# Performance work log

Measured on AMD Instinct MI355X. Metric: run time of the kernel, lower is better.

## Reference

```python
import jax, jax.numpy as jnp
import numpy as np

B, S, H = 8, 2048, 1024

def setup_inputs() -> dict:
    key = jax.random.key(0)
    k1, k2, k3 = jax.random.split(key, 3)
    lstm_out = jax.random.normal(k1, (B, S, H), dtype=jnp.float32)
    # nn.Linear(hidden_size, hidden_size): weight [H, H], bias [H]
    W = jax.random.normal(k2, (H, H), dtype=jnp.float32) * (1.0 / np.sqrt(H))
    b = jax.random.normal(k3, (H,), dtype=jnp.float32) * 0.01
    return {"lstm_out": lstm_out, "W": W, "b": b}

def reference(lstm_out, W, b):
    # out = linear(lstm_out)  (torch Linear: x @ W.T + b)
    out = jnp.einsum('bsh,oh->bso', lstm_out, W) + b            # [B,S,H]
    # score = bmm(out, out^T)  -- unscaled, Q = K
    score = jnp.einsum('bqh,bkh->bqk', out, out)                # [B,S,S]
    attn = jax.nn.softmax(score, axis=-1)                       # [B,S,S]
    # context = bmm(attn, lstm_out)
    context = jnp.einsum('bqk,bkh->bqh', attn, lstm_out)        # [B,S,H]
    return context
```

## Files before the change

### kernel.cpp

```cpp
#include <hip/hip_runtime.h>
#include <hip/hip_bf16.h>
#include <stdint.h>

#define BB 8
#define SS 2048
#define HH 1024

typedef __bf16 bf16_t;
typedef bf16_t bf16x8 __attribute__((ext_vector_type(8)));
typedef float f32x4 __attribute__((ext_vector_type(4)));
typedef unsigned short u16x8 __attribute__((ext_vector_type(8)));

__device__ __forceinline__ unsigned short f2bf(float f) {
    unsigned int u = __float_as_uint(f);
    u += 0x7fffu + ((u >> 16) & 1u);
    return (unsigned short)(u >> 16);
}

__global__ __launch_bounds__(256) void cast_f32_bf16(
    const float* __restrict__ in, unsigned short* __restrict__ out, int n4)
{
    int i = blockIdx.x * blockDim.x + threadIdx.x;
    int stride = gridDim.x * blockDim.x;
    for (; i < n4; i += stride) {
        float4 v = reinterpret_cast<const float4*>(in)[i];
        ushort4 o;
        o.x = f2bf(v.x); o.y = f2bf(v.y); o.z = f2bf(v.z); o.w = f2bf(v.w);
        reinterpret_cast<ushort4*>(out)[i] = o;
    }
}

__global__ __launch_bounds__(256) void transpose_cast(
    const float* __restrict__ in,
    unsigned short* __restrict__ outN,
    unsigned short* __restrict__ outT)
{
    __shared__ float tile[32][33];
    const int tx = threadIdx.x, ty = threadIdx.y;
    const int h0 = blockIdx.x * 32, s0 = blockIdx.y * 32, b = blockIdx.z;
    const float* src = in + ((size_t)b * SS + s0) * HH + h0;
    unsigned short* dN = outN + ((size_t)b * SS + s0) * HH + h0;
    unsigned short* dT = outT + ((size_t)b * HH + h0) * SS + s0;
#pragma unroll
    for (int i = 0; i < 4; i++) {
        float v = src[(size_t)(ty + i * 8) * HH + tx];
        tile[ty + i * 8][tx] = v;
        dN[(size_t)(ty + i * 8) * HH + tx] = f2bf(v);
    }
    __syncthreads();
#pragma unroll
    for (int i = 0; i < 4; i++) {
        dT[(size_t)(ty + i * 8) * SS + tx] = f2bf(tile[tx][ty + i * 8]);
    }
}

__global__ __launch_bounds__(256) void softmax_rows(float* __restrict__ score)
{
    const size_t row = blockIdx.x;
    float* srow = score + row * 2048;
    const int t = threadIdx.x;
    const int wave = t >> 6, lane = t & 63;

    float4 v0 = reinterpret_cast<float4*>(srow)[t * 2];
    float4 v1 = reinterpret_cast<float4*>(srow)[t * 2 + 1];
    float x[8] = {v0.x, v0.y, v0.z, v0.w, v1.x, v1.y, v1.z, v1.w};

    float m = x[0];
#pragma unroll
    for (int i = 1; i < 8; i++) m = fmaxf(m, x[i]);
#pragma unroll
    for (int off = 32; off; off >>= 1) m = fmaxf(m, __shfl_xor(m, off));

    __shared__ float red[4];
    if (!lane) red[wave] = m;
    __syncthreads();
    m = fmaxf(fmaxf(red[0], red[1]), fmaxf(red[2], red[3]));

    float e[8];
    float s = 0.0f;
#pragma unroll
    for (int i = 0; i < 8; i++) { e[i] = __expf(x[i] - m); s += e[i]; }
#pragma unroll
    for (int off = 32; off; off >>= 1) s += __shfl_xor(s, off);
    __syncthreads();
    if (!lane) red[wave] = s;
    __syncthreads();
    s = red[0] + red[1] + red[2] + red[3];
    const float inv = 1.0f / s;

    unsigned short* drow = reinterpret_cast<unsigned short*>(score) + row * 4096 + (size_t)t * 8;
    u16x8 o;
#pragma unroll
    for (int i = 0; i < 8; i++) o[i] = f2bf(e[i] * inv);
    *reinterpret_cast<u16x8*>(drow) = o;
}

#define GLL16(gp, lp)                                                        \
    __builtin_amdgcn_global_load_lds(                                        \
        (const __attribute__((address_space(1))) unsigned int*)(gp),         \
        (__attribute__((address_space(3))) unsigned int*)(lp), 16, 0, 0)

template <int OUT_BF16, int HAS_BIAS>
__global__ __launch_bounds__(256) void gemm_nt(
    const unsigned short* __restrict__ A, long long aBatch, int lda,
    const unsigned short* __restrict__ Bmat, long long bBatch, int ldb,
    void* __restrict__ Cp, long long cBatch, int ldc,
    const float* __restrict__ bias, int K)
{
    __shared__ unsigned short As[128 * 32];
    __shared__ unsigned short Bs[128 * 32];

    const int tid = threadIdx.x;
    const int wave = tid >> 6, lane = tid & 63;
    const int wr = wave >> 1, wc = wave & 1;
    const int fr = lane & 15;
    const int fk = (lane >> 4) * 8;

    const unsigned short* Ab = A + (size_t)blockIdx.z * aBatch
        + ((size_t)blockIdx.y * 128 + wave * 32 + (lane >> 2)) * lda + (lane & 3) * 8;
    const unsigned short* Bb = Bmat + (size_t)blockIdx.z * bBatch
        + ((size_t)blockIdx.x * 128 + wave * 32 + (lane >> 2)) * ldb + (lane & 3) * 8;
    unsigned short* lA0 = As + (wave * 32) * 32;
    unsigned short* lA1 = As + (wave * 32 + 16) * 32;
    unsigned short* lB0 = Bs + (wave * 32) * 32;
    unsigned short* lB1 = Bs + (wave * 32 + 16) * 32;
    const size_t a16 = (size_t)16 * lda, b16 = (size_t)16 * ldb;

    f32x4 acc[4][4];
    const f32x4 zero = {0.0f, 0.0f, 0.0f, 0.0f};
#pragma unroll
    for (int m = 0; m < 4; m++)
#pragma unroll
        for (int n = 0; n < 4; n++) acc[m][n] = zero;

    for (int k0 = 0; k0 < K; k0 += 32) {
        GLL16(Ab + k0, lA0);
        GLL16(Ab + k0 + a16, lA1);
        GLL16(Bb + k0, lB0);
        GLL16(Bb + k0 + b16, lB1);
        __syncthreads();

        bf16x8 aF[4], bF[4];
#pragma unroll
        for (int m = 0; m < 4; m++)
            aF[m] = *reinterpret_cast<const bf16x8*>(As + (wr * 64 + m * 16 + fr) * 32 + fk);
#pragma unroll
        for (int n = 0; n < 4; n++)
            bF[n] = *reinterpret_cast<const bf16x8*>(Bs + (wc * 64 + n * 16 + fr) * 32 + fk);
#pragma unroll
        for (int m = 0; m < 4; m++)
#pragma unroll
            for (int n = 0; n < 4; n++)
                acc[m][n] = __builtin_amdgcn_mfma_f32_16x16x32_bf16(aF[m], bF[n], acc[m][n], 0, 0, 0);
        __syncthreads();
    }

    const int rBase = blockIdx.y * 128 + wr * 64 + (lane >> 4) * 4;
    const int cBase = blockIdx.x * 128 + wc * 64 + fr;
    if (OUT_BF16) {
        unsigned short* C = (unsigned short*)Cp + (size_t)blockIdx.z * cBatch;
#pragma unroll
        for (int n = 0; n < 4; n++) {
            const int col = cBase + n * 16;
            const float bv = HAS_BIAS ? bias[col] : 0.0f;
#pragma unroll
            for (int m = 0; m < 4; m++) {
                const int row = rBase + m * 16;
#pragma unroll
                for (int j = 0; j < 4; j++)
                    C[(size_t)(row + j) * ldc + col] = f2bf(acc[m][n][j] + bv);
            }
        }
    } else {
        float* C = (float*)Cp + (size_t)blockIdx.z * cBatch;
#pragma unroll
        for (int n = 0; n < 4; n++) {
            const int col = cBase + n * 16;
#pragma unroll
            for (int m = 0; m < 4; m++) {
                const int row = rBase + m * 16;
#pragma unroll
                for (int j = 0; j < 4; j++)
                    C[(size_t)(row + j) * ldc + col] = acc[m][n][j];
            }
        }
    }
}

extern "C" void kernel_launch(void* const* d_in, const int* in_sizes, int n_in,
                              void* d_out, int out_size, void* d_ws, size_t ws_size,
                              hipStream_t stream)
{
    const float* lstm = (const float*)d_in[0];
    const float* W    = (const float*)d_in[1];
    const float* bias = (const float*)d_in[2];
    float* out = (float*)d_out;

    unsigned short* lstm_bf = (unsigned short*)d_ws;
    unsigned short* out_bf  = lstm_bf + (size_t)BB * SS * HH;
    unsigned short* lstmT   = out_bf + (size_t)BB * SS * HH;
    unsigned short* W_bf    = lstmT + (size_t)BB * HH * SS;
    float* score            = (float*)(W_bf + (size_t)HH * HH);

    transpose_cast<<<dim3(HH / 32, SS / 32, BB), dim3(32, 8), 0, stream>>>(
        lstm, lstm_bf, lstmT);

    cast_f32_bf16<<<dim3(512), dim3(256), 0, stream>>>(W, W_bf, HH * HH / 4);

    gemm_nt<1, 1><<<dim3(HH / 128, BB * SS / 128, 1), dim3(256), 0, stream>>>(
        lstm_bf, 0, HH, W_bf, 0, HH, out_bf, 0, HH, bias, HH);

    gemm_nt<0, 0><<<dim3(SS / 128, SS / 128, BB), dim3(256), 0, stream>>>(
        out_bf, (long long)SS * HH, HH,
        out_bf, (long long)SS * HH, HH,
        score, (long long)SS * SS, SS, nullptr, HH);

    softmax_rows<<<dim3(BB * SS), dim3(256), 0, stream>>>(score);

    gemm_nt<0, 0><<<dim3(HH / 128, SS / 128, BB), dim3(256), 0, stream>>>(
        (const unsigned short*)score, (long long)SS * 4096, 4096,
        lstmT, (long long)HH * SS, SS,
        out, (long long)SS * HH, HH, nullptr, SS);
}
```

Measured before the change: 428.2 us.

## Use 256x256 triple-buffered GEMM tiles and store scores in bf16

Replaces the 128x128 single-buffered GEMM with a 256x256-tile, 512-thread kernel. It uses triple-buffered LDS prefetch via global_load_lds, an XOR-swizzled LDS layout, split MFMA phases with setprio, and an XCD-aware workgroup remap. The score matrix is now written directly in bf16, which halves the score write and softmax read traffic. This trades score precision before softmax (bf16 logits can have large magnitude) and higher register/LDS pressure for better data reuse and load/compute overlap.

```diff
diff --git a/kernel.cpp b/kernel.cpp
--- a/kernel.cpp
+++ b/kernel.cpp
@@ -15,6 +15,9 @@
     unsigned int u = __float_as_uint(f);
     u += 0x7fffu + ((u >> 16) & 1u);
     return (unsigned short)(u >> 16);
+}
+__device__ __forceinline__ float bf2f(unsigned short h) {
+    return __uint_as_float((unsigned int)h << 16);
 }
 
 __global__ __launch_bounds__(256) void cast_f32_bf16(
@@ -54,16 +57,17 @@
     }
 }
 
-__global__ __launch_bounds__(256) void softmax_rows(float* __restrict__ score)
+__global__ __launch_bounds__(256) void softmax_rows_bf16(unsigned short* __restrict__ score)
 {
     const size_t row = blockIdx.x;
-    float* srow = score + row * 2048;
+    unsigned short* srow = score + row * 2048;
     const int t = threadIdx.x;
     const int wave = t >> 6, lane = t & 63;
 
-    float4 v0 = reinterpret_cast<float4*>(srow)[t * 2];
-    float4 v1 = reinterpret_cast<float4*>(srow)[t * 2 + 1];
-    float x[8] = {v0.x, v0.y, v0.z, v0.w, v1.x, v1.y, v1.z, v1.w};
+    u16x8 v = *reinterpret_cast<u16x8*>(srow + (size_t)t * 8);
+    float x[8];
+#pragma unroll
+    for (int i = 0; i < 8; i++) x[i] = bf2f(v[i]);
 
     float m = x[0];
 #pragma unroll
@@ -88,11 +92,10 @@
     s = red[0] + red[1] + red[2] + red[3];
     const float inv = 1.0f / s;
 
-    unsigned short* drow = reinterpret_cast<unsigned short*>(score) + row * 4096 + (size_t)t * 8;
     u16x8 o;
 #pragma unroll
     for (int i = 0; i < 8; i++) o[i] = f2bf(e[i] * inv);
-    *reinterpret_cast<u16x8*>(drow) = o;
+    *reinterpret_cast<u16x8*>(srow + (size_t)t * 8) = o;
 }
 
 #define GLL16(gp, lp)                                                        \
@@ -101,62 +104,116 @@
         (__attribute__((address_space(3))) unsigned int*)(lp), 16, 0, 0)
 
 template <int OUT_BF16, int HAS_BIAS>
-__global__ __launch_bounds__(256) void gemm_nt(
+__global__ __launch_bounds__(512, 2) void gemm_nt_256(
     const unsigned short* __restrict__ A, long long aBatch, int lda,
-    const unsigned short* __restrict__ Bmat, long long bBatch, int ldb,
+    const unsigned short* __restrict__ Bm, long long bBatch, int ldb,
     void* __restrict__ Cp, long long cBatch, int ldc,
-    const float* __restrict__ bias, int K)
-{
-    __shared__ unsigned short As[128 * 32];
-    __shared__ unsigned short Bs[128 * 32];
+    const float* __restrict__ bias, int K, int GXT)
+{
+    __shared__ unsigned short lds[3 * 16384];
 
     const int tid = threadIdx.x;
     const int wave = tid >> 6, lane = tid & 63;
-    const int wr = wave >> 1, wc = wave & 1;
-    const int fr = lane & 15;
-    const int fk = (lane >> 4) * 8;
-
-    const unsigned short* Ab = A + (size_t)blockIdx.z * aBatch
-        + ((size_t)blockIdx.y * 128 + wave * 32 + (lane >> 2)) * lda + (lane & 3) * 8;
-    const unsigned short* Bb = Bmat + (size_t)blockIdx.z * bBatch
-        + ((size_t)blockIdx.x * 128 + wave * 32 + (lane >> 2)) * ldb + (lane & 3) * 8;
-    unsigned short* lA0 = As + (wave * 32) * 32;
-    unsigned short* lA1 = As + (wave * 32 + 16) * 32;
-    unsigned short* lB0 = Bs + (wave * 32) * 32;
-    unsigned short* lB1 = Bs + (wave * 32 + 16) * 32;
-    const size_t a16 = (size_t)16 * lda, b16 = (size_t)16 * ldb;
-
-    f32x4 acc[4][4];
+    const int wr = wave >> 2, wc = wave & 3;
+    const int fr = lane & 15, fc = lane >> 4;
+
+    const int q = gridDim.x >> 3;
+    const int x = blockIdx.x;
+    const int wgid = (x & 7) * q + (x >> 3);
+    const int bx = wgid % GXT, by = wgid / GXT;
+
+    const unsigned short* Ap = A + (size_t)blockIdx.z * aBatch + (size_t)by * 256 * lda;
+    const unsigned short* Bp = Bm + (size_t)blockIdx.z * bBatch + (size_t)bx * 256 * ldb;
+
+    const int sr = tid >> 2;
+    const int sc = tid & 3;
+    const int r0 = sr, r1 = sr + 128;
+    const unsigned short* sA0 = Ap + (size_t)r0 * lda + ((sc ^ ((r0 >> 1) & 3)) << 3);
+    const unsigned short* sA1 = Ap + (size_t)r1 * lda + ((sc ^ ((r1 >> 1) & 3)) << 3);
+    const unsigned short* sB0 = Bp + (size_t)r0 * ldb + ((sc ^ ((r0 >> 1) & 3)) << 3);
+    const unsigned short* sB1 = Bp + (size_t)r1 * ldb + ((sc ^ ((r1 >> 1) & 3)) << 3);
+    const int dA0 = wave * 512;
+    const int dA1 = 4096 + wave * 512;
+
+    const int kch = ((fc ^ ((fr >> 1) & 3)) << 3);
+    int offA[8], offB[4];
+#pragma unroll
+    for (int m = 0; m < 8; m++) offA[m] = (wr * 128 + m * 16 + fr) * 32 + kch;
+#pragma unroll
+    for (int n = 0; n < 4; n++) offB[n] = (wc * 64 + n * 16 + fr) * 32 + kch;
+
+    f32x4 acc[8][4];
     const f32x4 zero = {0.0f, 0.0f, 0.0f, 0.0f};
 #pragma unroll
-    for (int m = 0; m < 4; m++)
+    for (int m = 0; m < 8; m++)
 #pragma unroll
         for (int n = 0; n < 4; n++) acc[m][n] = zero;
 
-    for (int k0 = 0; k0 < K; k0 += 32) {
-        GLL16(Ab + k0, lA0);
-        GLL16(Ab + k0 + a16, lA1);
-        GLL16(Bb + k0, lB0);
-        GLL16(Bb + k0 + b16, lB1);
-        __syncthreads();
-
-        bf16x8 aF[4], bF[4];
-#pragma unroll
-        for (int m = 0; m < 4; m++)
-            aF[m] = *reinterpret_cast<const bf16x8*>(As + (wr * 64 + m * 16 + fr) * 32 + fk);
+    const int NT = K >> 5;
+
+    {
+        unsigned short* b0 = lds;
+        unsigned short* b1 = lds + 16384;
+        GLL16(sA0, b0 + dA0); GLL16(sA1, b0 + dA1);
+        GLL16(sB0, b0 + 8192 + dA0); GLL16(sB1, b0 + 8192 + dA1);
+        GLL16(sA0 + 32, b1 + dA0); GLL16(sA1 + 32, b1 + dA1);
+        GLL16(sB0 + 32, b1 + 8192 + dA0); GLL16(sB1 + 32, b1 + 8192 + dA1);
+    }
+    asm volatile("s_waitcnt vmcnt(4)" ::: "memory");
+    __builtin_amdgcn_sched_barrier(0);
+    __builtin_amdgcn_s_barrier();
+
+    for (int t = 0; t < NT; ++t) {
+        const int cur = t % 3;
+        const int nb = (t + 2) % 3;
+        const int sk = (t + 2 < NT ? t + 2 : NT - 1) << 5;
+        const unsigned short* tA = lds + cur * 16384;
+        const unsigned short* tB = tA + 8192;
+        unsigned short* nA = lds + nb * 16384;
+        unsigned short* nB = nA + 8192;
+
+        bf16x8 a0[4], b0[4];
+#pragma unroll
+        for (int m = 0; m < 4; m++)
+            a0[m] = *reinterpret_cast<const bf16x8*>(tA + offA[m]);
 #pragma unroll
         for (int n = 0; n < 4; n++)
-            bF[n] = *reinterpret_cast<const bf16x8*>(Bs + (wc * 64 + n * 16 + fr) * 32 + fk);
+            b0[n] = *reinterpret_cast<const bf16x8*>(tB + offB[n]);
+        GLL16(sA0 + sk, nA + dA0);
+        GLL16(sA1 + sk, nA + dA1);
+        __builtin_amdgcn_s_barrier();
+        __builtin_amdgcn_s_setprio(1);
 #pragma unroll
         for (int m = 0; m < 4; m++)
 #pragma unroll
             for (int n = 0; n < 4; n++)
-                acc[m][n] = __builtin_amdgcn_mfma_f32_16x16x32_bf16(aF[m], bF[n], acc[m][n], 0, 0, 0);
-        __syncthreads();
-    }
-
-    const int rBase = blockIdx.y * 128 + wr * 64 + (lane >> 4) * 4;
-    const int cBase = blockIdx.x * 128 + wc * 64 + fr;
+                acc[m][n] = __builtin_amdgcn_mfma_f32_16x16x32_bf16(a0[m], b0[n], acc[m][n], 0, 0, 0);
+        __builtin_amdgcn_s_setprio(0);
+        __builtin_amdgcn_s_barrier();
+
+        bf16x8 a1[4];
+#pragma unroll
+        for (int m = 0; m < 4; m++)
+            a1[m] = *reinterpret_cast<const bf16x8*>(tA + offA[4 + m]);
+        GLL16(sB0 + sk, nB + dA0);
+        GLL16(sB1 + sk, nB + dA1);
+        __builtin_amdgcn_s_barrier();
+        __builtin_amdgcn_s_setprio(1);
+#pragma unroll
+        for (int m = 0; m < 4; m++)
+#pragma unroll
+            for (int n = 0; n < 4; n++)
+                acc[4 + m][n] = __builtin_amdgcn_mfma_f32_16x16x32_bf16(a1[m], b0[n], acc[4 + m][n], 0, 0, 0);
+        __builtin_amdgcn_s_setprio(0);
+        asm volatile("s_waitcnt vmcnt(4)" ::: "memory");
+        __builtin_amdgcn_sched_barrier(0);
+        __builtin_amdgcn_s_barrier();
+    }
+    asm volatile("s_waitcnt vmcnt(0)" ::: "memory");
+    __builtin_amdgcn_sched_barrier(0);
+
+    const int rBase = by * 256 + wr * 128 + fc * 4;
+    const int cBase = bx * 256 + wc * 64 + fr;
     if (OUT_BF16) {
         unsigned short* C = (unsigned short*)Cp + (size_t)blockIdx.z * cBatch;
 #pragma unroll
@@ -164,7 +221,7 @@
             const int col = cBase + n * 16;
             const float bv = HAS_BIAS ? bias[col] : 0.0f;
 #pragma unroll
-            for (int m = 0; m < 4; m++) {
+            for (int m = 0; m < 8; m++) {
                 const int row = rBase + m * 16;
 #pragma unroll
                 for (int j = 0; j < 4; j++)
@@ -177,7 +234,7 @@
         for (int n = 0; n < 4; n++) {
             const int col = cBase + n * 16;
 #pragma unroll
-            for (int m = 0; m < 4; m++) {
+            for (int m = 0; m < 8; m++) {
                 const int row = rBase + m * 16;
 #pragma unroll
                 for (int j = 0; j < 4; j++)
@@ -200,25 +257,25 @@
     unsigned short* out_bf  = lstm_bf + (size_t)BB * SS * HH;
     unsigned short* lstmT   = out_bf + (size_t)BB * SS * HH;
     unsigned short* W_bf    = lstmT + (size_t)BB * HH * SS;
-    float* score            = (float*)(W_bf + (size_t)HH * HH);
+    unsigned short* score   = W_bf + (size_t)HH * HH;
 
     transpose_cast<<<dim3(HH / 32, SS / 32, BB), dim3(32, 8), 0, stream>>>(
         lstm, lstm_bf, lstmT);
 
     cast_f32_bf16<<<dim3(512), dim3(256), 0, stream>>>(W, W_bf, HH * HH / 4);
 
-    gemm_nt<1, 1><<<dim3(HH / 128, BB * SS / 128, 1), dim3(256), 0, stream>>>(
-        lstm_bf, 0, HH, W_bf, 0, HH, out_bf, 0, HH, bias, HH);
-
-    gemm_nt<0, 0><<<dim3(SS / 128, SS / 128, BB), dim3(256), 0, stream>>>(
+    gemm_nt_256<1, 1><<<dim3(256, 1, 1), dim3(512), 0, stream>>>(
+        lstm_bf, 0, HH, W_bf, 0, HH, out_bf, 0, HH, bias, HH, HH / 256);
+
+    gemm_nt_256<1, 0><<<dim3(64, 1, BB), dim3(512), 0, stream>>>(
         out_bf, (long long)SS * HH, HH,
         out_bf, (long long)SS * HH, HH,
-        score, (long long)SS * SS, SS, nullptr, HH);
-
-    softmax_rows<<<dim3(BB * SS), dim3(256), 0, stream>>>(score);
-
-    gemm_nt<0, 0><<<dim3(HH / 128, SS / 128, BB), dim3(256), 0, stream>>>(
-        (const unsigned short*)score, (long long)SS * 4096, 4096,
+        score, (long long)SS * SS, SS, nullptr, HH, SS / 256);
+
+    softmax_rows_bf16<<<dim3(BB * SS), dim3(256), 0, stream>>>(score);
+
+    gemm_nt_256<0, 0><<<dim3(32, 1, BB), dim3(512), 0, stream>>>(
+        score, (long long)SS * SS, SS,
         lstmT, (long long)HH * SS, SS,
-        out, (long long)SS * HH, HH, nullptr, SS);
-}
+        out, (long long)SS * HH, HH, nullptr, SS, HH / 256);
+}
```

After: 349.5 us. 1.23x faster.
